# Optimization experiments

Measured on AMD Instinct MI355X. Metric: run time of the kernel, lower is better.

## Reference

```python
import jax, jax.numpy as jnp
import numpy as np

B, NI, NH = 1024, 32, 1024  # batch, num_inputs, num_hidden


def _masks(ni, nh):
    # get_mask semantics from the torch source (mask shape = (out_features, in_features))
    in_deg_input = jnp.arange(ni) % ni                # mask_type='input'
    hid_deg = jnp.arange(nh) % (ni - 1)               # hidden degrees
    out_deg_output = jnp.arange(2 * ni) % ni - 1      # mask_type='output'
    m1 = (hid_deg[:, None] >= in_deg_input[None, :]).astype(jnp.float32)   # (NH, NI)
    m2 = (hid_deg[:, None] >= hid_deg[None, :]).astype(jnp.float32)        # (NH, NH)
    m3 = (out_deg_output[:, None] >= hid_deg[None, :]).astype(jnp.float32) # (2*NI, NH)
    return m1, m2, m3


def setup_inputs() -> dict:
    key = jax.random.key(0)
    ks = jax.random.split(key, 7)
    s1 = 1.0 / np.sqrt(NI)
    s2 = 1.0 / np.sqrt(NH)
    return {
        "inputs": jax.random.normal(ks[0], (B, NI), dtype=jnp.float32),
        "W1": jax.random.normal(ks[1], (NH, NI), dtype=jnp.float32) * s1,
        "b1": jax.random.normal(ks[2], (NH,), dtype=jnp.float32) * s1,
        "W2": jax.random.normal(ks[3], (NH, NH), dtype=jnp.float32) * s2,
        "b2": jax.random.normal(ks[4], (NH,), dtype=jnp.float32) * s2,
        "W3": jax.random.normal(ks[5], (2 * NI, NH), dtype=jnp.float32) * s2,
        "b3": jax.random.normal(ks[6], (2 * NI,), dtype=jnp.float32) * s2,
    }


def reference(inputs, W1, b1, W2, b2, W3, b3):
    ni = inputs.shape[1]
    nh = W1.shape[0]
    m1, m2, m3 = _masks(ni, nh)
    M1, M2, M3 = W1 * m1, W2 * m2, W3 * m3  # masked weights, precomputed once

    def net(x):  # 3-layer masked MLP -> (B, 2*ni) params
        h = jax.nn.relu(x @ M1.T + b1)
        h = jax.nn.relu(h @ M2.T + b2)
        return h @ M3.T + b3

    def step(x, i):
        p = net(x)                       # (B, 2*ni)
        m_i = p[:, i]                    # mean for dim i
        a_i = jnp.tanh(p[:, ni + i])     # log-scale for dim i (use_tanh=True)
        x_i = inputs[:, i] * jnp.exp(a_i) + m_i
        return x.at[:, i].set(x_i), -a_i

    x, neg_a = jax.lax.scan(step, jnp.zeros_like(inputs), jnp.arange(ni))
    J = neg_a.sum(axis=0)[:, None]       # (B, 1)
    return x, J
```

## Files before the change

### kernel.cpp

```cpp
#include <hip/hip_runtime.h>
#include <math.h>

#define NI   32
#define NH   1024
#define NB   1024

#define OFF_B1S 0
#define OFF_B2S 1056
#define OFF_W3S 2080
#define OFF_W1B 67616
#define OFF_PB  84512

__device__ __forceinline__ int base_of(int d) { return (d == 0) ? 0 : 33 * d + 1; }

__device__ __forceinline__ unsigned short f2bf(float f) {
    unsigned u = __float_as_uint(f);
    return (unsigned short)((u + 0x7FFFu + ((u >> 16) & 1u)) >> 16);
}
__device__ __forceinline__ float bflo(unsigned u) { return __uint_as_float(u << 16); }
__device__ __forceinline__ float bfhi(unsigned u) { return __uint_as_float(u & 0xFFFF0000u); }

template <int CNT>
__device__ __forceinline__ void prep_w2_cls(int d, int oh0, const float* __restrict__ W2,
                                            unsigned short* __restrict__ pb16, int t,
                                            float (*tile)[65]) {
    const int bse = base_of(d);
#pragma unroll 1
    for (int e = t; e < CNT * 64; e += 256) {
        int k = e >> 6, c = e & 63;
        int og = d + 31 * k;
        tile[k][c] = W2[(size_t)og * NH + oh0 + c];
    }
    __syncthreads();
#pragma unroll 1
    for (int e = t; e < 64 * CNT; e += 256) {
        int oh_l = e / CNT;
        int k = e - oh_l * CNT;
        int oh = oh0 + oh_l;
        int dd = oh % 31, u = oh / 31;
        int sg = bse + k;
        float v = (d >= dd) ? tile[k][oh_l] : 0.0f;
        size_t a = (size_t)((dd * 17 + (u >> 1)) * 256 + (sg >> 2)) * 8
                 + (u & 1) * 4 + (sg & 3);
        pb16[a] = f2bf(v);
    }
}

template <int CNT>
__device__ __forceinline__ void prep_small_cls(int d, const float* __restrict__ W1,
        const float* __restrict__ b1, const float* __restrict__ b2,
        const float* __restrict__ W3, float* __restrict__ ws, int t) {
    const int bse = base_of(d);
    unsigned short* w1b16 = (unsigned short*)(ws + OFF_W1B);
#pragma unroll 1
    for (int e = t; e < 64 * CNT; e += 256) {
        int o = e / CNT, k = e - o * CNT;
        int og = d + 31 * k;
        float v = (((o & 31) - 1) >= d) ? W3[(size_t)o * NH + og] : 0.0f;
        ws[OFF_W3S + (size_t)o * NH + bse + k] = v;
    }
#pragma unroll 1
    for (int e = t; e < 32 * CNT; e += 256) {
        int j = e / CNT, k = e - j * CNT;
        int og = d + 31 * k;
        int su = bse + k;
        float v = (d >= j) ? W1[og * NI + j] : 0.0f;
        w1b16[(size_t)((j >> 1) * 1056 + su) * 2 + (j & 1)] = f2bf(v);
    }
    if (t < CNT) {
        int og = d + 31 * t;
        ws[OFF_B1S + bse + t] = b1[og];
        ws[OFF_B2S + bse + t] = b2[og];
    }
}

__global__ __launch_bounds__(256) void prep_all(const float* __restrict__ W1,
        const float* __restrict__ b1, const float* __restrict__ W2,
        const float* __restrict__ b2, const float* __restrict__ W3,
        float* __restrict__ ws) {
    __shared__ float tile[34][65];
    const int bid = blockIdx.x, t = threadIdx.x;
    unsigned short* pb16 = (unsigned short*)(ws + OFF_PB);
    if (bid < 496) {
        int d = bid >> 4, oh0 = (bid & 15) * 64;
        if (d == 0) prep_w2_cls<34>(0, oh0, W2, pb16, t, tile);
        else        prep_w2_cls<33>(d, oh0, W2, pb16, t, tile);
    } else {
        int d = bid - 496;
        if (d == 0) prep_small_cls<34>(0, W1, b1, b2, W3, ws, t);
        else        prep_small_cls<33>(d, W1, b1, b2, W3, ws, t);
    }
}

__device__ __forceinline__ void consume_pair(uint4 g, float4 av,
                                             float4& acc0, float4& acc1) {
    float f0 = bflo(g.x), f1 = bfhi(g.x), f2 = bflo(g.y), f3 = bfhi(g.y);
    float f4 = bflo(g.z), f5 = bfhi(g.z), f6 = bflo(g.w), f7 = bfhi(g.w);
    acc0.x = fmaf(av.x, f0, acc0.x); acc0.y = fmaf(av.x, f1, acc0.y);
    acc0.z = fmaf(av.x, f2, acc0.z); acc0.w = fmaf(av.x, f3, acc0.w);
    acc1.x = fmaf(av.y, f0, acc1.x); acc1.y = fmaf(av.y, f1, acc1.y);
    acc1.z = fmaf(av.y, f2, acc1.z); acc1.w = fmaf(av.y, f3, acc1.w);
    acc0.x = fmaf(av.z, f4, acc0.x); acc0.y = fmaf(av.z, f5, acc0.y);
    acc0.z = fmaf(av.z, f6, acc0.z); acc0.w = fmaf(av.z, f7, acc0.w);
    acc1.x = fmaf(av.w, f4, acc1.x); acc1.y = fmaf(av.w, f5, acc1.y);
    acc1.z = fmaf(av.w, f6, acc1.z); acc1.w = fmaf(av.w, f7, acc1.w);
}

__global__ __launch_bounds__(256, 2) void made_scan(
        const float* __restrict__ inputs,
        const float* __restrict__ b3,
        const float* __restrict__ ws,
        float* __restrict__ out) {
    __shared__ float xsS[4][2][36];
    __shared__ float a1S[4][36][2];
    __shared__ float part[2][4][4];
    __shared__ float b3S[64];
    __shared__ float xinS[2][NI];

    const int lane = threadIdx.x & 63;
    const int w    = threadIdx.x >> 6;
    const int pairity = ((blockIdx.x >> 8) ^ blockIdx.x) & 1;
    const int q    = w ^ (pairity * 3);
    const int gb   = q * 256;
    const int row0 = blockIdx.x * 2;

    const float* b1s = ws + OFF_B1S;
    const float* b2s = ws + OFF_B2S;
    const float* W3s = ws + OFF_W3S;
    const unsigned* W1B = (const unsigned*)(ws + OFF_W1B);
    const uint4*    PB  = (const uint4*)(ws + OFF_PB);

    float4 acc0 = ((const float4*)(b2s + gb))[lane];
    float4 acc1 = acc0;
    float J0 = 0.f, J1 = 0.f;

    if (w == 0) {
        b3S[lane] = b3[lane];
        if (lane < NI) {
            xinS[0][lane] = inputs[row0 * NI + lane];
            xinS[1][lane] = inputs[(row0 + 1) * NI + lane];
        }
    }
    {
        float* px = &xsS[w][0][0];
        for (int k = lane; k < 72; k += 64) px[k] = 0.f;
    }
    __syncthreads();

    {
        float p00 = b3S[0], p01 = b3S[NI];
        float e20 = __expf(2.f * fminf(p01, 15.f));
        float ta  = (e20 - 1.f) / (e20 + 1.f);
        float es  = __expf(ta);
        float x0  = fmaf(xinS[0][0], es, p00);
        float x1  = fmaf(xinS[1][0], es, p00);
        J0 -= ta; J1 -= ta;
        if (lane == 0) { xsS[w][0][0] = x0; xsS[w][1][0] = x1; }
    }

#pragma unroll 1
    for (int i = 1; i < NI; ++i) {
        const int dd   = i - 1;
        const int goff = base_of(dd);
        const int cnt  = (i == 1) ? 34 : 33;
        const bool doB = (gb + 256 > goff);
        const bool doC = (gb < 33 * i + 1);

        float4 wa = make_float4(0, 0, 0, 0), wb = make_float4(0, 0, 0, 0);
        if (doC) {
            wa = ((const float4*)(W3s + (size_t)i * NH + gb))[lane];
            wb = ((const float4*)(W3s + (size_t)(NI + i) * NH + gb))[lane];
        }

        if (doB) {
            const uint4* pbase = PB + (size_t)(dd * 17) * 256 + (gb >> 2) + lane;
            uint4 G1[9];
#pragma unroll
            for (int u2 = 0; u2 < 9; ++u2) G1[u2] = pbase[u2 * 256];
            __builtin_amdgcn_sched_barrier(0);

            const int su = goff + lane;
            float bz = b1s[su];
            unsigned wk[16];
#pragma unroll
            for (int k = 0; k < 16; ++k) wk[k] = W1B[k * 1056 + su];
            float zA0 = bz, zA1 = 0, zA2 = 0, zA3 = 0;
            float zB0 = bz, zB1 = 0, zB2 = 0, zB3 = 0;
#pragma unroll
            for (int j4 = 0; j4 < 8; ++j4) {
                float4 xq0 = *(const float4*)&xsS[w][0][4 * j4];
                float4 xq1 = *(const float4*)&xsS[w][1][4 * j4];
                float w0 = bflo(wk[2 * j4]),     w1 = bfhi(wk[2 * j4]);
                float w2 = bflo(wk[2 * j4 + 1]), w3 = bfhi(wk[2 * j4 + 1]);
                zA0 = fmaf(xq0.x, w0, zA0); zB0 = fmaf(xq1.x, w0, zB0);
                zA1 = fmaf(xq0.y, w1, zA1); zB1 = fmaf(xq1.y, w1, zB1);
                zA2 = fmaf(xq0.z, w2, zA2); zB2 = fmaf(xq1.z, w2, zB2);
                zA3 = fmaf(xq0.w, w3, zA3); zB3 = fmaf(xq1.w, w3, zB3);
            }
            const bool ok = lane < cnt;
            float a0 = ok ? fmaxf((zA0 + zA1) + (zA2 + zA3), 0.f) : 0.f;
            float a1 = ok ? fmaxf((zB0 + zB1) + (zB2 + zB3), 0.f) : 0.f;
            if (lane < 36) {
                float2 v = make_float2(a0, a1);
                *(float2*)&a1S[w][lane][0] = v;
            }
            __builtin_amdgcn_sched_barrier(0);

            uint4 G2[8];
#pragma unroll
            for (int u2 = 0; u2 < 8; ++u2) G2[u2] = pbase[(9 + u2) * 256];
            __builtin_amdgcn_sched_barrier(0);
#pragma unroll
            for (int u2 = 0; u2 < 9; ++u2)
                consume_pair(G1[u2], *(const float4*)&a1S[w][2 * u2][0], acc0, acc1);
            __builtin_amdgcn_sched_barrier(0);
#pragma unroll
            for (int u2 = 0; u2 < 8; ++u2)
                consume_pair(G2[u2], *(const float4*)&a1S[w][18 + 2 * u2][0], acc0, acc1);
        }

        float s00 = 0, s01 = 0, s10 = 0, s11 = 0;
        if (doC) {
            float hx, hy, hz, hw;
            hx = fmaxf(acc0.x, 0.f); hy = fmaxf(acc0.y, 0.f);
            hz = fmaxf(acc0.z, 0.f); hw = fmaxf(acc0.w, 0.f);
            s00 = fmaf(wa.x, hx, fmaf(wa.y, hy, fmaf(wa.z, hz, wa.w * hw)));
            s01 = fmaf(wb.x, hx, fmaf(wb.y, hy, fmaf(wb.z, hz, wb.w * hw)));
            hx = fmaxf(acc1.x, 0.f); hy = fmaxf(acc1.y, 0.f);
            hz = fmaxf(acc1.z, 0.f); hw = fmaxf(acc1.w, 0.f);
            s10 = fmaf(wa.x, hx, fmaf(wa.y, hy, fmaf(wa.z, hz, wa.w * hw)));
            s11 = fmaf(wb.x, hx, fmaf(wb.y, hy, fmaf(wb.z, hz, wb.w * hw)));
#pragma unroll
            for (int m = 32; m >= 1; m >>= 1) {
                s00 += __shfl_xor(s00, m, 64); s01 += __shfl_xor(s01, m, 64);
                s10 += __shfl_xor(s10, m, 64); s11 += __shfl_xor(s11, m, 64);
            }
        }
        if (lane == 0)
            *((float4*)&part[i & 1][w][0]) = make_float4(s00, s01, s10, s11);
        __syncthreads();

        const float* pb = &part[i & 1][0][0];
        float4 q0 = ((const float4*)pb)[0], q1 = ((const float4*)pb)[1];
        float4 q2 = ((const float4*)pb)[2], q3 = ((const float4*)pb)[3];
        float bi  = b3S[i];
        float bia = b3S[NI + i];
        float p00 = ((q0.x + q1.x) + (q2.x + q3.x)) + bi;
        float p01 = ((q0.y + q1.y) + (q2.y + q3.y)) + bia;
        float p10 = ((q0.z + q1.z) + (q2.z + q3.z)) + bi;
        float p11 = ((q0.w + q1.w) + (q2.w + q3.w)) + bia;
        float e20 = __expf(2.f * fminf(p01, 15.f));
        float ta0 = (e20 - 1.f) / (e20 + 1.f);
        float x0  = fmaf(xinS[0][i], __expf(ta0), p00);
        float e21 = __expf(2.f * fminf(p11, 15.f));
        float ta1 = (e21 - 1.f) / (e21 + 1.f);
        float x1  = fmaf(xinS[1][i], __expf(ta1), p10);
        J0 -= ta0; J1 -= ta1;
        if (lane == 0) { xsS[w][0][i] = x0; xsS[w][1][i] = x1; }
    }

    if (w == 0) {
        if (lane < NI) {
            out[row0 * NI + lane]       = xsS[0][0][lane];
            out[(row0 + 1) * NI + lane] = xsS[0][1][lane];
        }
        if (lane == 0) {
            out[NB * NI + row0]     = J0;
            out[NB * NI + row0 + 1] = J1;
        }
    }
}

extern "C" void kernel_launch(void* const* d_in, const int* in_sizes, int n_in,
                              void* d_out, int out_size, void* d_ws, size_t ws_size,
                              hipStream_t stream) {
    const float* inputs = (const float*)d_in[0];
    const float* W1     = (const float*)d_in[1];
    const float* b1     = (const float*)d_in[2];
    const float* W2     = (const float*)d_in[3];
    const float* b2     = (const float*)d_in[4];
    const float* W3     = (const float*)d_in[5];
    const float* b3     = (const float*)d_in[6];
    float* out = (float*)d_out;
    float* ws  = (float*)d_ws;

    prep_all<<<527, 256, 0, stream>>>(W1, b1, W2, b2, W3, ws);
    made_scan<<<NB / 2, 256, 0, stream>>>(inputs, b3, ws, out);
}
```

Measured before the change: 166.6 us.

## Process one batch row per block instead of two, doubling block count

```diff
diff --git a/kernel.cpp b/kernel.cpp
--- a/kernel.cpp
+++ b/kernel.cpp
@@ -92,37 +92,32 @@
     }
 }
 
-__device__ __forceinline__ void consume_pair(uint4 g, float4 av,
-                                             float4& acc0, float4& acc1) {
+__device__ __forceinline__ void consume_pair1(uint4 g, float2 av, float4& acc) {
     float f0 = bflo(g.x), f1 = bfhi(g.x), f2 = bflo(g.y), f3 = bfhi(g.y);
     float f4 = bflo(g.z), f5 = bfhi(g.z), f6 = bflo(g.w), f7 = bfhi(g.w);
-    acc0.x = fmaf(av.x, f0, acc0.x); acc0.y = fmaf(av.x, f1, acc0.y);
-    acc0.z = fmaf(av.x, f2, acc0.z); acc0.w = fmaf(av.x, f3, acc0.w);
-    acc1.x = fmaf(av.y, f0, acc1.x); acc1.y = fmaf(av.y, f1, acc1.y);
-    acc1.z = fmaf(av.y, f2, acc1.z); acc1.w = fmaf(av.y, f3, acc1.w);
-    acc0.x = fmaf(av.z, f4, acc0.x); acc0.y = fmaf(av.z, f5, acc0.y);
-    acc0.z = fmaf(av.z, f6, acc0.z); acc0.w = fmaf(av.z, f7, acc0.w);
-    acc1.x = fmaf(av.w, f4, acc1.x); acc1.y = fmaf(av.w, f5, acc1.y);
-    acc1.z = fmaf(av.w, f6, acc1.z); acc1.w = fmaf(av.w, f7, acc1.w);
-}
-
-__global__ __launch_bounds__(256, 2) void made_scan(
+    acc.x = fmaf(av.x, f0, acc.x); acc.y = fmaf(av.x, f1, acc.y);
+    acc.z = fmaf(av.x, f2, acc.z); acc.w = fmaf(av.x, f3, acc.w);
+    acc.x = fmaf(av.y, f4, acc.x); acc.y = fmaf(av.y, f5, acc.y);
+    acc.z = fmaf(av.y, f6, acc.z); acc.w = fmaf(av.y, f7, acc.w);
+}
+
+__global__ __launch_bounds__(256, 4) void made_scan(
         const float* __restrict__ inputs,
         const float* __restrict__ b3,
         const float* __restrict__ ws,
         float* __restrict__ out) {
-    __shared__ float xsS[4][2][36];
-    __shared__ float a1S[4][36][2];
-    __shared__ float part[2][4][4];
+    __shared__ float xsS[4][36];
+    __shared__ float a1S[4][40];
+    __shared__ float part[2][4][2];
     __shared__ float b3S[64];
-    __shared__ float xinS[2][NI];
+    __shared__ float xinS[NI];
 
     const int lane = threadIdx.x & 63;
     const int w    = threadIdx.x >> 6;
-    const int pairity = ((blockIdx.x >> 8) ^ blockIdx.x) & 1;
-    const int q    = w ^ (pairity * 3);
+    const int rot  = (blockIdx.x + (blockIdx.x >> 8)) & 3;
+    const int q    = (w + rot) & 3;
     const int gb   = q * 256;
-    const int row0 = blockIdx.x * 2;
+    const int row  = blockIdx.x;
 
     const float* b1s = ws + OFF_B1S;
     const float* b2s = ws + OFF_B2S;
@@ -130,32 +125,23 @@
     const unsigned* W1B = (const unsigned*)(ws + OFF_W1B);
     const uint4*    PB  = (const uint4*)(ws + OFF_PB);
 
-    float4 acc0 = ((const float4*)(b2s + gb))[lane];
-    float4 acc1 = acc0;
-    float J0 = 0.f, J1 = 0.f;
+    float4 acc = ((const float4*)(b2s + gb))[lane];
+    float J = 0.f;
 
     if (w == 0) {
         b3S[lane] = b3[lane];
-        if (lane < NI) {
-            xinS[0][lane] = inputs[row0 * NI + lane];
-            xinS[1][lane] = inputs[(row0 + 1) * NI + lane];
-        }
-    }
-    {
-        float* px = &xsS[w][0][0];
-        for (int k = lane; k < 72; k += 64) px[k] = 0.f;
-    }
+        if (lane < NI) xinS[lane] = inputs[row * NI + lane];
+    }
+    if (lane < 36) xsS[w][lane] = 0.f;
     __syncthreads();
 
     {
         float p00 = b3S[0], p01 = b3S[NI];
         float e20 = __expf(2.f * fminf(p01, 15.f));
         float ta  = (e20 - 1.f) / (e20 + 1.f);
-        float es  = __expf(ta);
-        float x0  = fmaf(xinS[0][0], es, p00);
-        float x1  = fmaf(xinS[1][0], es, p00);
-        J0 -= ta; J1 -= ta;
-        if (lane == 0) { xsS[w][0][0] = x0; xsS[w][1][0] = x1; }
+        float x0  = fmaf(xinS[0], __expf(ta), p00);
+        J -= ta;
+        if (lane == 0) xsS[w][0] = x0;
     }
 
 #pragma unroll 1
@@ -184,26 +170,20 @@
             unsigned wk[16];
 #pragma unroll
             for (int k = 0; k < 16; ++k) wk[k] = W1B[k * 1056 + su];
-            float zA0 = bz, zA1 = 0, zA2 = 0, zA3 = 0;
-            float zB0 = bz, zB1 = 0, zB2 = 0, zB3 = 0;
+            float z0 = bz, z1 = 0, z2 = 0, z3 = 0;
 #pragma unroll
             for (int j4 = 0; j4 < 8; ++j4) {
-                float4 xq0 = *(const float4*)&xsS[w][0][4 * j4];
-                float4 xq1 = *(const float4*)&xsS[w][1][4 * j4];
+                float4 xq = *(const float4*)&xsS[w][4 * j4];
                 float w0 = bflo(wk[2 * j4]),     w1 = bfhi(wk[2 * j4]);
                 float w2 = bflo(wk[2 * j4 + 1]), w3 = bfhi(wk[2 * j4 + 1]);
-                zA0 = fmaf(xq0.x, w0, zA0); zB0 = fmaf(xq1.x, w0, zB0);
-                zA1 = fmaf(xq0.y, w1, zA1); zB1 = fmaf(xq1.y, w1, zB1);
-                zA2 = fmaf(xq0.z, w2, zA2); zB2 = fmaf(xq1.z, w2, zB2);
-                zA3 = fmaf(xq0.w, w3, zA3); zB3 = fmaf(xq1.w, w3, zB3);
+                z0 = fmaf(xq.x, w0, z0);
+                z1 = fmaf(xq.y, w1, z1);
+                z2 = fmaf(xq.z, w2, z2);
+                z3 = fmaf(xq.w, w3, z3);
             }
             const bool ok = lane < cnt;
-            float a0 = ok ? fmaxf((zA0 + zA1) + (zA2 + zA3), 0.f) : 0.f;
-            float a1 = ok ? fmaxf((zB0 + zB1) + (zB2 + zB3), 0.f) : 0.f;
-            if (lane < 36) {
-                float2 v = make_float2(a0, a1);
-                *(float2*)&a1S[w][lane][0] = v;
-            }
+            float a0 = ok ? fmaxf((z0 + z1) + (z2 + z3), 0.f) : 0.f;
+            if (lane < 36) a1S[w][lane] = a0;
             __builtin_amdgcn_sched_barrier(0);
 
             uint4 G2[8];
@@ -212,62 +192,45 @@
             __builtin_amdgcn_sched_barrier(0);
 #pragma unroll
             for (int u2 = 0; u2 < 9; ++u2)
-                consume_pair(G1[u2], *(const float4*)&a1S[w][2 * u2][0], acc0, acc1);
+                consume_pair1(G1[u2], *(const float2*)&a1S[w][2 * u2], acc);
             __builtin_amdgcn_sched_barrier(0);
 #pragma unroll
             for (int u2 = 0; u2 < 8; ++u2)
-                consume_pair(G2[u2], *(const float4*)&a1S[w][18 + 2 * u2][0], acc0, acc1);
+                consume_pair1(G2[u2], *(const float2*)&a1S[w][18 + 2 * u2], acc);
         }
 
-        float s00 = 0, s01 = 0, s10 = 0, s11 = 0;
+        float s00 = 0, s01 = 0;
         if (doC) {
-            float hx, hy, hz, hw;
-            hx = fmaxf(acc0.x, 0.f); hy = fmaxf(acc0.y, 0.f);
-            hz = fmaxf(acc0.z, 0.f); hw = fmaxf(acc0.w, 0.f);
+            float hx = fmaxf(acc.x, 0.f), hy = fmaxf(acc.y, 0.f);
+            float hz = fmaxf(acc.z, 0.f), hw = fmaxf(acc.w, 0.f);
             s00 = fmaf(wa.x, hx, fmaf(wa.y, hy, fmaf(wa.z, hz, wa.w * hw)));
             s01 = fmaf(wb.x, hx, fmaf(wb.y, hy, fmaf(wb.z, hz, wb.w * hw)));
-            hx = fmaxf(acc1.x, 0.f); hy = fmaxf(acc1.y, 0.f);
-            hz = fmaxf(acc1.z, 0.f); hw = fmaxf(acc1.w, 0.f);
-            s10 = fmaf(wa.x, hx, fmaf(wa.y, hy, fmaf(wa.z, hz, wa.w * hw)));
-            s11 = fmaf(wb.x, hx, fmaf(wb.y, hy, fmaf(wb.z, hz, wb.w * hw)));
 #pragma unroll
             for (int m = 32; m >= 1; m >>= 1) {
-                s00 += __shfl_xor(s00, m, 64); s01 += __shfl_xor(s01, m, 64);
-                s10 += __shfl_xor(s10, m, 64); s11 += __shfl_xor(s11, m, 64);
+                s00 += __shfl_xor(s00, m, 64);
+                s01 += __shfl_xor(s01, m, 64);
             }
         }
         if (lane == 0)
-            *((float4*)&part[i & 1][w][0]) = make_float4(s00, s01, s10, s11);
+            *((float2*)&part[i & 1][w][0]) = make_float2(s00, s01);
         __syncthreads();
 
         const float* pb = &part[i & 1][0][0];
         float4 q0 = ((const float4*)pb)[0], q1 = ((const float4*)pb)[1];
-        float4 q2 = ((const float4*)pb)[2], q3 = ((const float4*)pb)[3];
         float bi  = b3S[i];
         float bia = b3S[NI + i];
-        float p00 = ((q0.x + q1.x) + (q2.x + q3.x)) + bi;
-        float p01 = ((q0.y + q1.y) + (q2.y + q3.y)) + bia;
-        float p10 = ((q0.z + q1.z) + (q2.z + q3.z)) + bi;
-        float p11 = ((q0.w + q1.w) + (q2.w + q3.w)) + bia;
+        float p00 = ((q0.x + q0.z) + (q1.x + q1.z)) + bi;
+        float p01 = ((q0.y + q0.w) + (q1.y + q1.w)) + bia;
         float e20 = __expf(2.f * fminf(p01, 15.f));
         float ta0 = (e20 - 1.f) / (e20 + 1.f);
-        float x0  = fmaf(xinS[0][i], __expf(ta0), p00);
-        float e21 = __expf(2.f * fminf(p11, 15.f));
-        float ta1 = (e21 - 1.f) / (e21 + 1.f);
-        float x1  = fmaf(xinS[1][i], __expf(ta1), p10);
-        J0 -= ta0; J1 -= ta1;
-        if (lane == 0) { xsS[w][0][i] = x0; xsS[w][1][i] = x1; }
+        float x0  = fmaf(xinS[i], __expf(ta0), p00);
+        J -= ta0;
+        if (lane == 0) xsS[w][i] = x0;
     }
 
     if (w == 0) {
-        if (lane < NI) {
-            out[row0 * NI + lane]       = xsS[0][0][lane];
-            out[(row0 + 1) * NI + lane] = xsS[0][1][lane];
-        }
-        if (lane == 0) {
-            out[NB * NI + row0]     = J0;
-            out[NB * NI + row0 + 1] = J1;
-        }
+        if (lane < NI) out[row * NI + lane] = xsS[0][lane];
+        if (lane == 0) out[NB * NI + row] = J;
     }
 }
 
@@ -285,5 +248,5 @@
     float* ws  = (float*)d_ws;
 
     prep_all<<<527, 256, 0, stream>>>(W1, b1, W2, b2, W3, ws);
-    made_scan<<<NB / 2, 256, 0, stream>>>(inputs, b3, ws, out);
-}
+    made_scan<<<NB, 256, 0, stream>>>(inputs, b3, ws, out);
+}
```

Result: slower. 194.3 us (+16.6%).
